# Performance work log

Hardware: AMD Instinct MI355X
Metric: run time of the kernel (lower is better)

## Reference

```python
import jax, jax.numpy as jnp
import numpy as np

V, E, H, T, L = 100000, 300, 256, 5, 8192  # vocab, embed, hidden(per dir), tags, seq_len


def setup_inputs() -> dict:
    key = jax.random.key(0)
    ks = jax.random.split(key, 16)
    sentence = jax.random.randint(ks[0], (L,), 1, V)
    embed = jax.random.normal(ks[1], (V, E), jnp.float32) * 0.1
    embed = embed.at[0].set(0.0)  # padding_idx=0
    s = float(1.0 / np.sqrt(H))
    u = lambda k, shape: jax.random.uniform(k, shape, jnp.float32, -s, s)
    W_ih_f = u(ks[2], (4 * H, E)); W_hh_f = u(ks[3], (4 * H, H)); b_f = u(ks[4], (4 * H,))
    W_ih_b = u(ks[5], (4 * H, E)); W_hh_b = u(ks[6], (4 * H, H)); b_b = u(ks[7], (4 * H,))
    h0 = jax.random.normal(ks[8], (2, H), jnp.float32)  # init_h uses randn
    c0 = jax.random.normal(ks[9], (2, H), jnp.float32)
    W_out = u(ks[10], (T, 2 * H)); b_out = u(ks[11], (T,))
    start = jax.random.normal(ks[12], (T,), jnp.float32) * 0.1
    end = jax.random.normal(ks[13], (T,), jnp.float32) * 0.1
    trans = jax.random.normal(ks[14], (T, T), jnp.float32) * 0.1  # trans[i,j]: i -> j
    return dict(sentence=sentence, embed=embed, W_ih_f=W_ih_f, W_hh_f=W_hh_f, b_f=b_f,
                W_ih_b=W_ih_b, W_hh_b=W_hh_b, b_b=b_b, h0=h0, c0=c0,
                W_out=W_out, b_out=b_out, start=start, end=end, trans=trans)


def _lstm_dir(x, W_ih, W_hh, b, h0, c0, reverse):
    # x: [L, E]; precompute input projection outside the scan
    xproj = x @ W_ih.T + b  # [L, 4H]
    def step(carry, xp):
        h, c = carry
        g = xp + h @ W_hh.T
        i, f, gg, o = jnp.split(g, 4)
        i = jax.nn.sigmoid(i); f = jax.nn.sigmoid(f)
        gg = jnp.tanh(gg); o = jax.nn.sigmoid(o)
        c = f * c + i * gg
        h = o * jnp.tanh(c)
        return (h, c), h
    _, hs = jax.lax.scan(step, (h0, c0), xproj, reverse=reverse)
    return hs  # [L, H], aligned with input time order


def _viterbi(emission, start, end, trans):
    # emission: [L, T]. CRF Viterbi decode (torchcrf semantics, batch=1).
    score0 = start + emission[0]
    def step(score, em):
        cand = score[:, None] + trans + em[None, :]  # [T_prev, T_next]
        return jnp.max(cand, axis=0), jnp.argmax(cand, axis=0)
    score, bps = jax.lax.scan(step, score0, emission[1:])
    last = jnp.argmax(score + end)
    def back(tag, bp):
        prev = bp[tag]
        return prev, prev
    _, path = jax.lax.scan(back, last, bps, reverse=True)
    return jnp.concatenate([path, last[None]])  # [L] best tag sequence


def reference(sentence, embed, W_ih_f, W_hh_f, b_f, W_ih_b, W_hh_b, b_b,
              h0, c0, W_out, b_out, start, end, trans):
    x = embed[sentence]  # [L, E] embedding gather
    hf = _lstm_dir(x, W_ih_f, W_hh_f, b_f, h0[0], c0[0], False)
    hb = _lstm_dir(x, W_ih_b, W_hh_b, b_b, h0[1], c0[1], True)
    h = jnp.concatenate([hf, hb], axis=-1)  # [L, 2H]
    emission = h @ W_out.T + b_out  # [L, T]
    return _viterbi(emission, start, end, trans)
```

## Files before the change

### kernel.cpp

```cpp
#include <hip/hip_runtime.h>

#define L  8192
#define E  300
#define H  256
#define FH 1024
#define T  5

#define NCH 64
#define CHL 128
#define WUP 48

typedef float f32x4 __attribute__((ext_vector_type(4)));

#define XP_OFF   0u
#define HS_OFF   16777216u
#define EM_OFF   20971520u
#define PC_OFF   21037312u
#define SB_OFF   21039360u
#define LAST_OFF 21039880u
#define BP_BYTE  84159552u
#define F_BYTE   84200512u
#define TB_BYTE  84201024u
#define WR_BYTE  84205568u

__device__ __forceinline__ float red8(float x) {
  x += __int_as_float(__builtin_amdgcn_update_dpp(0, __float_as_int(x), 0xB1, 0xF, 0xF, true));
  x += __int_as_float(__builtin_amdgcn_update_dpp(0, __float_as_int(x), 0x4E, 0xF, 0xF, true));
  x += __int_as_float(__builtin_amdgcn_update_dpp(0, __float_as_int(x), 0x141, 0xF, 0xF, true));
  return x;
}

__global__ __launch_bounds__(256) void k_xproj(
    const int* __restrict__ sent, const float* __restrict__ embed,
    const float* __restrict__ wihf, const float* __restrict__ bf,
    const float* __restrict__ wihb, const float* __restrict__ bb,
    float* __restrict__ xp)
{
  __shared__ float xl[32][304];
  __shared__ int sl[32];
  const int tid = threadIdx.x;
  const int t0 = blockIdx.x * 32;
  const int d = blockIdx.y >> 1, rh = blockIdx.y & 1;
  const int r1 = rh * 256 + tid;
  const int r2 = r1 + 512;
  if (tid < 32) sl[tid] = sent[t0 + tid];
  __syncthreads();
  for (int tt = 0; tt < 32; ++tt) {
    const float* erow = embed + (size_t)sl[tt] * 300;
    for (int kk = tid; kk < 300; kk += 256) xl[tt][kk] = erow[kk];
  }
  __syncthreads();
  const float* wih  = d ? wihb : wihf;
  const float* bias = d ? bb : bf;
  const float4* wra = (const float4*)(wih + (size_t)r1 * 300);
  const float4* wrb = (const float4*)(wih + (size_t)r2 * 300);
  float acca[32], accb[32];
#pragma unroll
  for (int tt = 0; tt < 32; ++tt) { acca[tt] = 0.f; accb[tt] = 0.f; }
  for (int k4 = 0; k4 < 75; ++k4) {
    const float4 wa = wra[k4];
    const float4 wb = wrb[k4];
#pragma unroll
    for (int tt = 0; tt < 32; ++tt) {
      const float4 xv = *(const float4*)&xl[tt][k4 * 4];
      acca[tt] = fmaf(wa.x, xv.x, fmaf(wa.y, xv.y, fmaf(wa.z, xv.z, fmaf(wa.w, xv.w, acca[tt]))));
      accb[tt] = fmaf(wb.x, xv.x, fmaf(wb.y, xv.y, fmaf(wb.z, xv.z, fmaf(wb.w, xv.w, accb[tt]))));
    }
  }
  const float bv1 = bias[r1], bv2 = bias[r2];
#pragma unroll
  for (int tt = 0; tt < 32; ++tt) {
    xp[((size_t)d * L + (t0 + tt)) * FH + r1] = acca[tt] + bv1;
    xp[((size_t)d * L + (t0 + tt)) * FH + r2] = accb[tt] + bv2;
  }
}

__global__ __launch_bounds__(512, 2) void k_lstm(
    const float* __restrict__ xp,
    const float* __restrict__ whhf, const float* __restrict__ whhb,
    const float* __restrict__ h0, const float* __restrict__ c0,
    float* __restrict__ hs, float* __restrict__ wring)
{
  const int bid = blockIdx.x;
  const int gid = bid & 31;
  const int g   = bid >> 5;
  const int d = gid >> 4, p = gid & 15;
  const int kA = 4 * p, kB = 4 * p + 1, kC = 4 * p + 2, kD = 4 * p + 3;
  const int tid = threadIdx.x;
  const int l = tid & 63, w = tid >> 6;
  const int ul = w * 8 + (l >> 3);
  const int j  = g * 64 + ul;
  const int kq = l & 7;
  const float* whh = d ? whhb : whhf;

  float wgf[4][32];
#pragma unroll
  for (int gt = 0; gt < 4; ++gt) {
    const float* base = whh + (size_t)(gt * 256 + j) * 256 + kq * 32;
#pragma unroll
    for (int i = 0; i < 8; ++i) {
      float4 v = *(const float4*)(base + 4 * i);
      asm volatile("" : "+v"(v.x), "+v"(v.y), "+v"(v.z), "+v"(v.w));
      wgf[gt][4 * i + 0] = v.x; wgf[gt][4 * i + 1] = v.y;
      wgf[gt][4 * i + 2] = v.z; wgf[gt][4 * i + 3] = v.w;
    }
  }

  __shared__ float lh[4][2][256];
  __shared__ int lfl[4];
  __shared__ int ldone[4];
  if (tid < 4) { lfl[tid] = 0; ldone[tid] = 0; }
  __syncthreads();

  const bool noWA = (d == 0 && kA == 0);
  const bool noWD = (d == 1 && kD == NCH - 1);
  float cA = noWA ? c0[d * 256 + j] : 0.f;
  float cB = 0.f;
  float cC = 0.f;
  float cD = noWD ? c0[d * 256 + j] : 0.f;

  float* ringA = wring + (size_t)(d * NCH + kA) * (WUP * 256);
  float* ringB = wring + (size_t)(d * NCH + kB) * (WUP * 256);
  float* ringC = wring + (size_t)(d * NCH + kC) * (WUP * 256);
  float* ringD = wring + (size_t)(d * NCH + kD) * (WUP * 256);

  bool slow = false;

  auto chunk_step = [&](int ci, int kch, bool noW, float* ring, float& cst, int r) {
    const int Wc = noW ? 0 : WUP;
    const int sc = noW ? (r - WUP) : r;
    if (sc < 0 || sc >= Wc + CHL) return;
    const int t = d ? (kch * CHL + CHL - 1 + Wc - sc)
                    : (kch * CHL - Wc + sc);

    const float* xr = xp + ((size_t)d * L + t) * FH;
    const float x0 = xr[j], x1 = xr[256 + j], x2 = xr[512 + j], x3 = xr[768 + j];

    float a0 = 0.f, a1 = 0.f, a2 = 0.f, a3 = 0.f;
    if (sc == 0) {
      if (noW) {
        const float* hp = h0 + d * 256 + kq * 32;
#pragma unroll
        for (int ii = 0; ii < 8; ++ii) {
          const f32x4 hc = *(const f32x4*)(hp + 4 * ii);
#pragma unroll
          for (int dd = 0; dd < 4; ++dd) {
            const float hv = hc[dd];
            a0 = fmaf(wgf[0][4 * ii + dd], hv, a0);
            a1 = fmaf(wgf[1][4 * ii + dd], hv, a1);
            a2 = fmaf(wgf[2][4 * ii + dd], hv, a2);
            a3 = fmaf(wgf[3][4 * ii + dd], hv, a3);
          }
        }
      }
    } else {
      if (w == 0) {
        if (sc >= 2) {
          while (__hip_atomic_load(&ldone[ci], __ATOMIC_RELAXED,
                                   __HIP_MEMORY_SCOPE_WORKGROUP) < 8 * (sc - 1)) {}
        }
        const float* src = (sc - 1 < Wc)
            ? (ring + (size_t)(sc - 1) * 256)
            : (hs + ((size_t)d * L + (d ? t + 1 : t - 1)) * H);
        const float* myp = src + 4 * l;
        f32x4 hx;
        int iters = 0;
        for (;;) {
          if (!slow) {
            asm volatile("global_load_dwordx4 %0, %1, off sc0\n\t"
                         "s_waitcnt vmcnt(0)"
                         : "=v"(hx) : "v"(myp) : "memory");
          } else {
            asm volatile("s_sleep 8\n\t"
                         "global_load_dwordx4 %0, %1, off sc0 sc1\n\t"
                         "s_waitcnt vmcnt(0)"
                         : "=v"(hx) : "v"(myp) : "memory");
          }
          const unsigned u0 = __float_as_uint(hx.x), u1 = __float_as_uint(hx.y);
          const unsigned u2 = __float_as_uint(hx.z), u3 = __float_as_uint(hx.w);
          const bool bad = (u0 == 0xFFFFFFFFu) | (u1 == 0xFFFFFFFFu) |
                           (u2 == 0xFFFFFFFFu) | (u3 == 0xFFFFFFFFu);
          if (!__any(bad)) break;
          if (!slow && ++iters > 4096) slow = true;
        }
        const int rr = l >> 3, cc = l & 7;
        *(f32x4*)&lh[ci][sc & 1][rr * 32 + 4 * (cc ^ rr)] = hx;
        asm volatile("s_waitcnt lgkmcnt(0)" ::: "memory");
        __hip_atomic_store(&lfl[ci], sc, __ATOMIC_RELAXED, __HIP_MEMORY_SCOPE_WORKGROUP);
      } else {
        while (__hip_atomic_load(&lfl[ci], __ATOMIC_RELAXED,
                                 __HIP_MEMORY_SCOPE_WORKGROUP) < sc) {}
      }
#pragma unroll
      for (int ii = 0; ii < 8; ++ii) {
        const f32x4 hc = *(const f32x4*)&lh[ci][sc & 1][kq * 32 + 4 * (ii ^ kq)];
#pragma unroll
        for (int dd = 0; dd < 4; ++dd) {
          const float hv = hc[dd];
          a0 = fmaf(wgf[0][4 * ii + dd], hv, a0);
          a1 = fmaf(wgf[1][4 * ii + dd], hv, a1);
          a2 = fmaf(wgf[2][4 * ii + dd], hv, a2);
          a3 = fmaf(wgf[3][4 * ii + dd], hv, a3);
        }
      }
    }
    a0 = red8(a0); a1 = red8(a1); a2 = red8(a2); a3 = red8(a3);

    const float gi = x0 + a0, gf = x1 + a1, gc = x2 + a2, go = x3 + a3;
    const float ig = 1.f / (1.f + __expf(-gi));
    const float fg = 1.f / (1.f + __expf(-gf));
    const float cg = 1.f - 2.f / (1.f + __expf(2.f * gc));
    const float og = 1.f / (1.f + __expf(-go));
    cst = fg * cst + ig * cg;
    const float hn = og * (1.f - 2.f / (1.f + __expf(2.f * cst)));
    if (kq == 0) {
      float* dst = (sc < Wc) ? (ring + (size_t)sc * 256 + j)
                             : (hs + ((size_t)d * L + t) * H + j);
      asm volatile("global_store_dword %0, %1, off sc0"
                   :: "v"(dst), "v"(hn) : "memory");
    }
    if (l == 0)
      __hip_atomic_fetch_add(&ldone[ci], 1, __ATOMIC_RELAXED, __HIP_MEMORY_SCOPE_WORKGROUP);
  };

  for (int r = 0; r < WUP + CHL; ++r) {
    chunk_step(0, kA, noWA, ringA, cA, r);
    chunk_step(1, kB, false, ringB, cB, r);
    chunk_step(2, kC, false, ringC, cC, r);
    chunk_step(3, kD, noWD, ringD, cD, r);
    if ((r & 63) == 63) __threadfence();
  }
}

__global__ __launch_bounds__(256) void k_emis(
    const float* __restrict__ hs, const float* __restrict__ wout,
    const float* __restrict__ bout, float* __restrict__ em)
{
  const int tid = threadIdx.x, l = tid & 63;
  const int t = blockIdx.x * 4 + (tid >> 6);
  const float4 hf = ((const float4*)(hs + (size_t)t * H))[l];
  const float4 hb = ((const float4*)(hs + (size_t)L * H + (size_t)t * H))[l];
  const float4* w4 = (const float4*)wout;
  float s[5];
#pragma unroll
  for (int tag = 0; tag < 5; ++tag) {
    const float4 wf = w4[tag * 128 + l];
    const float4 wb = w4[tag * 128 + 64 + l];
    float p = hf.x * wf.x + hf.y * wf.y + hf.z * wf.z + hf.w * wf.w
            + hb.x * wb.x + hb.y * wb.y + hb.z * wb.z + hb.w * wb.w;
#pragma unroll
    for (int m = 1; m < 64; m <<= 1) p += __shfl_xor(p, m, 64);
    s[tag] = p;
  }
  if (l == 0) {
#pragma unroll
    for (int tag = 0; tag < 5; ++tag) em[(size_t)t * 8 + tag] = s[tag] + bout[tag];
  }
}

__global__ __launch_bounds__(64) void k_v1(const float* __restrict__ em,
    const float* __restrict__ trans, float* __restrict__ pc)
{
  const int c = blockIdx.x, l = threadIdx.x;
  const int ii = l / 5, jj = l % 5;
  const float tc0 = trans[0 * 5 + jj], tc1 = trans[1 * 5 + jj], tc2 = trans[2 * 5 + jj];
  const float tc3 = trans[3 * 5 + jj], tc4 = trans[4 * 5 + jj];
  const int t0 = c * 128 + 1;
  const int t1 = min(t0 + 127, L - 1);
  float M = ((ii < 5) ? trans[ii * 5 + jj] : 0.f) + em[(size_t)t0 * 8 + jj];
  for (int t = t0 + 1; t <= t1; ++t) {
    const float emj = em[(size_t)t * 8 + jj];
    const float m0 = __shfl(M, ii * 5 + 0, 64) + tc0;
    const float m1 = __shfl(M, ii * 5 + 1, 64) + tc1;
    const float m2 = __shfl(M, ii * 5 + 2, 64) + tc2;
    const float m3 = __shfl(M, ii * 5 + 3, 64) + tc3;
    const float m4 = __shfl(M, ii * 5 + 4, 64) + tc4;
    M = fmaxf(fmaxf(fmaxf(m0, m1), fmaxf(m2, m3)), m4) + emj;
  }
  if (l < 25) pc[c * 32 + l] = M;
}

__global__ __launch_bounds__(64) void k_v2(const float* __restrict__ em,
    const float* __restrict__ pc, const float* __restrict__ start_,
    const float* __restrict__ end_, float* __restrict__ sb, int* __restrict__ last_)
{
  __shared__ float lpc[2048];
  const int l = threadIdx.x;
  for (int i = l; i < 2048; i += 64) lpc[i] = pc[i];
  __syncthreads();
  const int jj = (l < 5) ? l : 0;
  float s = start_[jj] + em[jj];
  if (l < 5) sb[l] = s;
  for (int c = 0; c < 64; ++c) {
    const float s0 = __shfl(s, 0, 64), s1 = __shfl(s, 1, 64), s2 = __shfl(s, 2, 64);
    const float s3 = __shfl(s, 3, 64), s4 = __shfl(s, 4, 64);
    s = fmaxf(fmaxf(fmaxf(s0 + lpc[c * 32 + 0 * 5 + jj], s1 + lpc[c * 32 + 1 * 5 + jj]),
                    fmaxf(s2 + lpc[c * 32 + 2 * 5 + jj], s3 + lpc[c * 32 + 3 * 5 + jj])),
              s4 + lpc[c * 32 + 4 * 5 + jj]);
    if (l < 5) sb[(c + 1) * 8 + l] = s;
  }
  const float v = s + end_[jj];
  const float v0 = __shfl(v, 0, 64), v1 = __shfl(v, 1, 64), v2 = __shfl(v, 2, 64);
  const float v3 = __shfl(v, 3, 64), v4 = __shfl(v, 4, 64);
  if (l == 0) {
    float best = v0; int bt = 0;
    if (v1 > best) { best = v1; bt = 1; }
    if (v2 > best) { best = v2; bt = 2; }
    if (v3 > best) { best = v3; bt = 3; }
    if (v4 > best) { best = v4; bt = 4; }
    *last_ = bt;
  }
}

__global__ __launch_bounds__(64) void k_v3(const float* __restrict__ em,
    const float* __restrict__ trans, const float* __restrict__ sb,
    unsigned char* __restrict__ bp)
{
  const int c = blockIdx.x, l = threadIdx.x;
  const int jj = (l < 5) ? l : 0;
  const float tc0 = trans[0 * 5 + jj], tc1 = trans[1 * 5 + jj], tc2 = trans[2 * 5 + jj];
  const float tc3 = trans[3 * 5 + jj], tc4 = trans[4 * 5 + jj];
  float s = sb[c * 8 + jj];
  const int t0 = c * 128 + 1, t1 = min(c * 128 + 128, L - 1);
  for (int t = t0; t <= t1; ++t) {
    const float s0 = __shfl(s, 0, 64), s1 = __shfl(s, 1, 64), s2 = __shfl(s, 2, 64);
    const float s3 = __shfl(s, 3, 64), s4 = __shfl(s, 4, 64);
    float best = s0 + tc0; int bi = 0;
    float cv = s1 + tc1; if (cv > best) { best = cv; bi = 1; }
    cv = s2 + tc2; if (cv > best) { best = cv; bi = 2; }
    cv = s3 + tc3; if (cv > best) { best = cv; bi = 3; }
    cv = s4 + tc4; if (cv > best) { best = cv; bi = 4; }
    if (l < 5) bp[(size_t)t * 5 + jj] = (unsigned char)bi;
    s = best + em[(size_t)t * 8 + jj];
  }
}

__global__ __launch_bounds__(64) void k_v4(const unsigned char* __restrict__ bp,
    unsigned char* __restrict__ F)
{
  __shared__ unsigned char bl[128 * 5];
  const int c = blockIdx.x, l = threadIdx.x;
  const int t0 = c * 128 + 1, t1 = min(c * 128 + 128, L - 1);
  const int n = t1 - t0 + 1;
  for (int i = l; i < n * 5; i += 64) bl[i] = bp[(size_t)t0 * 5 + i];
  __syncthreads();
  if (l < 5) {
    int tag = l;
    for (int t = t1; t >= t0; --t) tag = bl[(t - t0) * 5 + tag];
    F[c * 8 + l] = (unsigned char)tag;
  }
}

__global__ __launch_bounds__(64) void k_v5(const unsigned char* __restrict__ F,
    const int* __restrict__ last_, int* __restrict__ tb)
{
  __shared__ unsigned char lf[512];
  const int l = threadIdx.x;
  for (int i = l; i < 512; i += 64) lf[i] = F[i];
  __syncthreads();
  if (l == 0) {
    int cur = *last_;
    for (int c = 63; c >= 0; --c) { cur = lf[c * 8 + cur]; tb[c] = cur; }
  }
}

__global__ __launch_bounds__(64) void k_v6(const unsigned char* __restrict__ bp,
    const int* __restrict__ tb, const int* __restrict__ last_, int* __restrict__ out)
{
  __shared__ unsigned char bl[128 * 5];
  const int c = blockIdx.x, l = threadIdx.x;
  const int t0 = c * 128 + 1, t1 = min(c * 128 + 128, L - 1);
  const int n = t1 - t0 + 1;
  for (int i = l; i < n * 5; i += 64) bl[i] = bp[(size_t)t0 * 5 + i];
  __syncthreads();
  if (l == 0) {
    int cur = (c == 63) ? *last_ : tb[c + 1];
    if (c == 63) out[L - 1] = cur;
    for (int t = t1; t >= t0; --t) { cur = bl[(t - t0) * 5 + cur]; out[t - 1] = cur; }
  }
}

extern "C" void kernel_launch(void* const* d_in, const int* in_sizes, int n_in,
                              void* d_out, int out_size, void* d_ws, size_t ws_size,
                              hipStream_t stream)
{
  const int*   sent   = (const int*)d_in[0];
  const float* embed  = (const float*)d_in[1];
  const float* wihf   = (const float*)d_in[2];
  const float* whhf   = (const float*)d_in[3];
  const float* bf     = (const float*)d_in[4];
  const float* wihb   = (const float*)d_in[5];
  const float* whhb   = (const float*)d_in[6];
  const float* bb     = (const float*)d_in[7];
  const float* h0     = (const float*)d_in[8];
  const float* c0     = (const float*)d_in[9];
  const float* wout   = (const float*)d_in[10];
  const float* bout   = (const float*)d_in[11];
  const float* start_ = (const float*)d_in[12];
  const float* end_   = (const float*)d_in[13];
  const float* trans  = (const float*)d_in[14];

  float* ws   = (float*)d_ws;
  float* xp   = ws + XP_OFF;
  float* hs   = ws + HS_OFF;
  float* em   = ws + EM_OFF;
  float* pc   = ws + PC_OFF;
  float* sb   = ws + SB_OFF;
  int*   last_ = (int*)(ws + LAST_OFF);
  unsigned char* bp = (unsigned char*)d_ws + BP_BYTE;
  unsigned char* F  = (unsigned char*)d_ws + F_BYTE;
  int* tb = (int*)((unsigned char*)d_ws + TB_BYTE);
  float* wring = (float*)((unsigned char*)d_ws + WR_BYTE);
  int* out = (int*)d_out;

  hipMemsetAsync(hs, 0xFF, (size_t)4194304 * 4, stream);
  hipMemsetAsync(wring, 0xFF, (size_t)128 * WUP * 256 * 4, stream);
  k_xproj<<<dim3(256, 4), 256, 0, stream>>>(sent, embed, wihf, bf, wihb, bb, xp);
  k_lstm <<<128, 512, 0, stream>>>(xp, whhf, whhb, h0, c0, hs, wring);
  k_emis <<<2048, 256, 0, stream>>>(hs, wout, bout, em);
  k_v1   <<<64, 64, 0, stream>>>(em, trans, pc);
  k_v2   <<<1, 64, 0, stream>>>(em, pc, start_, end_, sb, last_);
  k_v3   <<<64, 64, 0, stream>>>(em, trans, sb, bp);
  k_v4   <<<64, 64, 0, stream>>>(bp, F);
  k_v5   <<<1, 64, 0, stream>>>(F, last_, tb);
  k_v6   <<<64, 64, 0, stream>>>(bp, tb, last_, out);
}
```

Measured before the change: 1.031 ms.

## Spread LSTM hidden-state polling across waves and double xproj time tile

```diff
diff --git a/kernel.cpp b/kernel.cpp
--- a/kernel.cpp
+++ b/kernel.cpp
@@ -36,16 +36,16 @@
     const float* __restrict__ wihb, const float* __restrict__ bb,
     float* __restrict__ xp)
 {
-  __shared__ float xl[32][304];
-  __shared__ int sl[32];
+  __shared__ float xl[64][304];
+  __shared__ int sl[64];
   const int tid = threadIdx.x;
-  const int t0 = blockIdx.x * 32;
+  const int t0 = blockIdx.x * 64;
   const int d = blockIdx.y >> 1, rh = blockIdx.y & 1;
   const int r1 = rh * 256 + tid;
   const int r2 = r1 + 512;
-  if (tid < 32) sl[tid] = sent[t0 + tid];
-  __syncthreads();
-  for (int tt = 0; tt < 32; ++tt) {
+  if (tid < 64) sl[tid] = sent[t0 + tid];
+  __syncthreads();
+  for (int tt = 0; tt < 64; ++tt) {
     const float* erow = embed + (size_t)sl[tt] * 300;
     for (int kk = tid; kk < 300; kk += 256) xl[tt][kk] = erow[kk];
   }
@@ -54,14 +54,14 @@
   const float* bias = d ? bb : bf;
   const float4* wra = (const float4*)(wih + (size_t)r1 * 300);
   const float4* wrb = (const float4*)(wih + (size_t)r2 * 300);
-  float acca[32], accb[32];
-#pragma unroll
-  for (int tt = 0; tt < 32; ++tt) { acca[tt] = 0.f; accb[tt] = 0.f; }
+  float acca[64], accb[64];
+#pragma unroll
+  for (int tt = 0; tt < 64; ++tt) { acca[tt] = 0.f; accb[tt] = 0.f; }
   for (int k4 = 0; k4 < 75; ++k4) {
     const float4 wa = wra[k4];
     const float4 wb = wrb[k4];
 #pragma unroll
-    for (int tt = 0; tt < 32; ++tt) {
+    for (int tt = 0; tt < 64; ++tt) {
       const float4 xv = *(const float4*)&xl[tt][k4 * 4];
       acca[tt] = fmaf(wa.x, xv.x, fmaf(wa.y, xv.y, fmaf(wa.z, xv.z, fmaf(wa.w, xv.w, acca[tt]))));
       accb[tt] = fmaf(wb.x, xv.x, fmaf(wb.y, xv.y, fmaf(wb.z, xv.z, fmaf(wb.w, xv.w, accb[tt]))));
@@ -69,7 +69,7 @@
   }
   const float bv1 = bias[r1], bv2 = bias[r2];
 #pragma unroll
-  for (int tt = 0; tt < 32; ++tt) {
+  for (int tt = 0; tt < 64; ++tt) {
     xp[((size_t)d * L + (t0 + tt)) * FH + r1] = acca[tt] + bv1;
     xp[((size_t)d * L + (t0 + tt)) * FH + r2] = accb[tt] + bv2;
   }
@@ -106,7 +106,7 @@
     }
   }
 
-  __shared__ float lh[4][2][256];
+  __shared__ float lh[4][4][256];
   __shared__ int lfl[4];
   __shared__ int ldone[4];
   if (tid < 4) { lfl[tid] = 0; ldone[tid] = 0; }
@@ -125,14 +125,56 @@
   float* ringD = wring + (size_t)(d * NCH + kD) * (WUP * 256);
 
   bool slow = false;
-
-  auto chunk_step = [&](int ci, int kch, bool noW, float* ring, float& cst, int r) {
+  const int rr = l >> 3, cc = l & 7;
+
+  auto duty_acquire = [&](int ci, int kch, bool noW, float* ring, int r) {
+    const int Wc = noW ? 0 : WUP;
+    const int sc = noW ? (r - WUP) : r;
+    if (sc < 1 || sc >= Wc + CHL) return;
+    if (sc >= 4) {
+      while (__hip_atomic_load(&ldone[ci], __ATOMIC_RELAXED,
+                               __HIP_MEMORY_SCOPE_WORKGROUP) < 8 * (sc - 3)) {}
+    }
+    const float* src;
+    if (sc - 1 < Wc) {
+      src = ring + (size_t)(sc - 1) * 256;
+    } else {
+      const int tp = d ? (kch * CHL + CHL - 1 + Wc - (sc - 1))
+                       : (kch * CHL - Wc + (sc - 1));
+      src = hs + ((size_t)d * L + tp) * H;
+    }
+    const float* myp = src + 4 * l;
+    f32x4 hx;
+    int iters = 0;
+    for (;;) {
+      if (!slow) {
+        asm volatile("global_load_dwordx4 %0, %1, off sc0\n\t"
+                     "s_waitcnt vmcnt(0)"
+                     : "=v"(hx) : "v"(myp) : "memory");
+      } else {
+        asm volatile("s_sleep 8\n\t"
+                     "global_load_dwordx4 %0, %1, off sc0 sc1\n\t"
+                     "s_waitcnt vmcnt(0)"
+                     : "=v"(hx) : "v"(myp) : "memory");
+      }
+      const unsigned u0 = __float_as_uint(hx.x), u1 = __float_as_uint(hx.y);
+      const unsigned u2 = __float_as_uint(hx.z), u3 = __float_as_uint(hx.w);
+      const bool bad = (u0 == 0xFFFFFFFFu) | (u1 == 0xFFFFFFFFu) |
+                       (u2 == 0xFFFFFFFFu) | (u3 == 0xFFFFFFFFu);
+      if (!__any(bad)) break;
+      if (!slow && ++iters > 4096) slow = true;
+    }
+    *(f32x4*)&lh[ci][sc & 3][rr * 32 + 4 * (cc ^ rr)] = hx;
+    asm volatile("s_waitcnt lgkmcnt(0)" ::: "memory");
+    __hip_atomic_store(&lfl[ci], sc, __ATOMIC_RELAXED, __HIP_MEMORY_SCOPE_WORKGROUP);
+  };
+
+  auto chunk_compute = [&](int ci, int kch, bool noW, float* ring, float& cst, int r) {
     const int Wc = noW ? 0 : WUP;
     const int sc = noW ? (r - WUP) : r;
     if (sc < 0 || sc >= Wc + CHL) return;
     const int t = d ? (kch * CHL + CHL - 1 + Wc - sc)
                     : (kch * CHL - Wc + sc);
-
     const float* xr = xp + ((size_t)d * L + t) * FH;
     const float x0 = xr[j], x1 = xr[256 + j], x2 = xr[512 + j], x3 = xr[768 + j];
 
@@ -154,46 +196,13 @@
         }
       }
     } else {
-      if (w == 0) {
-        if (sc >= 2) {
-          while (__hip_atomic_load(&ldone[ci], __ATOMIC_RELAXED,
-                                   __HIP_MEMORY_SCOPE_WORKGROUP) < 8 * (sc - 1)) {}
-        }
-        const float* src = (sc - 1 < Wc)
-            ? (ring + (size_t)(sc - 1) * 256)
-            : (hs + ((size_t)d * L + (d ? t + 1 : t - 1)) * H);
-        const float* myp = src + 4 * l;
-        f32x4 hx;
-        int iters = 0;
-        for (;;) {
-          if (!slow) {
-            asm volatile("global_load_dwordx4 %0, %1, off sc0\n\t"
-                         "s_waitcnt vmcnt(0)"
-                         : "=v"(hx) : "v"(myp) : "memory");
-          } else {
-            asm volatile("s_sleep 8\n\t"
-                         "global_load_dwordx4 %0, %1, off sc0 sc1\n\t"
-                         "s_waitcnt vmcnt(0)"
-                         : "=v"(hx) : "v"(myp) : "memory");
-          }
-          const unsigned u0 = __float_as_uint(hx.x), u1 = __float_as_uint(hx.y);
-          const unsigned u2 = __float_as_uint(hx.z), u3 = __float_as_uint(hx.w);
-          const bool bad = (u0 == 0xFFFFFFFFu) | (u1 == 0xFFFFFFFFu) |
-                           (u2 == 0xFFFFFFFFu) | (u3 == 0xFFFFFFFFu);
-          if (!__any(bad)) break;
-          if (!slow && ++iters > 4096) slow = true;
-        }
-        const int rr = l >> 3, cc = l & 7;
-        *(f32x4*)&lh[ci][sc & 1][rr * 32 + 4 * (cc ^ rr)] = hx;
-        asm volatile("s_waitcnt lgkmcnt(0)" ::: "memory");
-        __hip_atomic_store(&lfl[ci], sc, __ATOMIC_RELAXED, __HIP_MEMORY_SCOPE_WORKGROUP);
-      } else {
+      if (w != ci) {
         while (__hip_atomic_load(&lfl[ci], __ATOMIC_RELAXED,
                                  __HIP_MEMORY_SCOPE_WORKGROUP) < sc) {}
       }
 #pragma unroll
       for (int ii = 0; ii < 8; ++ii) {
-        const f32x4 hc = *(const f32x4*)&lh[ci][sc & 1][kq * 32 + 4 * (ii ^ kq)];
+        const f32x4 hc = *(const f32x4*)&lh[ci][sc & 3][kq * 32 + 4 * (ii ^ kq)];
 #pragma unroll
         for (int dd = 0; dd < 4; ++dd) {
           const float hv = hc[dd];
@@ -224,10 +233,14 @@
   };
 
   for (int r = 0; r < WUP + CHL; ++r) {
-    chunk_step(0, kA, noWA, ringA, cA, r);
-    chunk_step(1, kB, false, ringB, cB, r);
-    chunk_step(2, kC, false, ringC, cC, r);
-    chunk_step(3, kD, noWD, ringD, cD, r);
+    if      (w == 0) duty_acquire(0, kA, noWA, ringA, r);
+    else if (w == 1) duty_acquire(1, kB, false, ringB, r);
+    else if (w == 2) duty_acquire(2, kC, false, ringC, r);
+    else if (w == 3) duty_acquire(3, kD, noWD, ringD, r);
+    chunk_compute(0, kA, noWA, ringA, cA, r);
+    chunk_compute(1, kB, false, ringB, cB, r);
+    chunk_compute(2, kC, false, ringC, cC, r);
+    chunk_compute(3, kD, noWD, ringD, cD, r);
     if ((r & 63) == 63) __threadfence();
   }
 }
@@ -415,7 +428,7 @@
 
   hipMemsetAsync(hs, 0xFF, (size_t)4194304 * 4, stream);
   hipMemsetAsync(wring, 0xFF, (size_t)128 * WUP * 256 * 4, stream);
-  k_xproj<<<dim3(256, 4), 256, 0, stream>>>(sent, embed, wihf, bf, wihb, bb, xp);
+  k_xproj<<<dim3(128, 4), 256, 0, stream>>>(sent, embed, wihf, bf, wihb, bb, xp);
   k_lstm <<<128, 512, 0, stream>>>(xp, whhf, whhb, h0, c0, hs, wring);
   k_emis <<<2048, 256, 0, stream>>>(hs, wout, bout, em);
   k_v1   <<<64, 64, 0, stream>>>(em, trans, pc);
```

After: 3.141 ms. +204.7%, slower.
